# Optimization experiments

Measured on AMD Instinct MI355X. Metric: run time of the kernel, lower is better.

The kernel has to match this reference:

```python
import jax, jax.numpy as jnp
import numpy as np

DIM = 768
N_HEADS = 12
HEAD_DIM = DIM // N_HEADS
HIDDEN = 4 * DIM
EPS = 1e-5


def _layernorm(x, g, b):
    m = jnp.mean(x, axis=-1, keepdims=True)
    v = jnp.mean(jnp.square(x - m), axis=-1, keepdims=True)
    return (x - m) * jax.lax.rsqrt(v + EPS) * g + b


def setup_inputs() -> dict:
    key = jax.random.key(0)
    ks = jax.random.split(key, 16)
    s = lambda fan_in: 1.0 / np.sqrt(fan_in)
    return {
        "x": jax.random.normal(ks[0], (2, 2048, DIM), dtype=jnp.float32),
        "ln1_g": jnp.ones((DIM,), jnp.float32),
        "ln1_b": jnp.zeros((DIM,), jnp.float32),
        "qkv_w": jax.random.uniform(ks[1], (DIM, 3 * DIM), jnp.float32, -s(DIM), s(DIM)),
        "qkv_b": jax.random.uniform(ks[2], (3 * DIM,), jnp.float32, -s(DIM), s(DIM)),
        "proj_w": jax.random.uniform(ks[3], (DIM, DIM), jnp.float32, -s(DIM), s(DIM)),
        "proj_b": jax.random.uniform(ks[4], (DIM,), jnp.float32, -s(DIM), s(DIM)),
        "ln2_g": jnp.ones((DIM,), jnp.float32),
        "ln2_b": jnp.zeros((DIM,), jnp.float32),
        "w1": jax.random.uniform(ks[5], (DIM, HIDDEN), jnp.float32, -s(DIM), s(DIM)),
        "b1": jax.random.uniform(ks[6], (HIDDEN,), jnp.float32, -s(DIM), s(DIM)),
        "w2": jax.random.uniform(ks[7], (HIDDEN, DIM), jnp.float32, -s(HIDDEN), s(HIDDEN)),
        "b2": jax.random.uniform(ks[8], (DIM,), jnp.float32, -s(HIDDEN), s(HIDDEN)),
    }


def reference(x, ln1_g, ln1_b, qkv_w, qkv_b, proj_w, proj_b, ln2_g, ln2_b, w1, b1, w2, b2):
    B, N, C = x.shape
    # ---- attention branch (pre-norm) ----
    h = _layernorm(x, ln1_g, ln1_b)
    qkv = (h @ qkv_w + qkv_b).reshape(B, N, 3, N_HEADS, HEAD_DIM)
    qkv = qkv.transpose(2, 0, 3, 1, 4)  # [3, B, H, N, Dh]
    q, k, v = qkv[0], qkv[1], qkv[2]
    scale = HEAD_DIM ** -0.5
    scores = jnp.einsum("bhnd,bhmd->bhnm", q, k) * scale  # [B,H,N,N]
    attn = jax.nn.softmax(scores, axis=-1)
    ctx = jnp.einsum("bhnm,bhmd->bhnd", attn, v)  # [B,H,N,Dh]
    ctx = ctx.transpose(0, 2, 1, 3).reshape(B, N, C)
    x = x + ctx @ proj_w + proj_b
    # ---- MLP branch (pre-norm) ----
    h = _layernorm(x, ln2_g, ln2_b)
    h = jax.nn.gelu(h @ w1 + b1, approximate=False)  # torch nn.GELU default = exact erf
    x = x + h @ w2 + b2
    return x
```

## Files before the change

kernel.cpp:

```cpp
#include <hip/hip_runtime.h>
#include <hip/hip_bf16.h>
#include <math.h>

#define DIM 768
#define NHEADS 12
#define HDIM 64
#define HIDDEN 3072
#define SEQ 2048
#define NTOK 4096
#define QKV3 2304

typedef __attribute__((ext_vector_type(8))) __bf16 bf16x8;
typedef __attribute__((ext_vector_type(4))) float f32x4;
typedef __attribute__((ext_vector_type(16))) float f32x16;

__device__ __forceinline__ ushort f32_bf16(float f) {
  union { float f; uint u; } c{f};
  uint u = c.u;
  u = (u + 0x7FFFu + ((u >> 16) & 1u)) >> 16;
  return (ushort)u;
}

__device__ __forceinline__ float bf16_f32(ushort u) {
  union { uint u; float f; } c{(uint)u << 16};
  return c.f;
}

__device__ __forceinline__ uint cvt_pk_bf16(float lo, float hi) {
  uint r;
  asm("v_cvt_pk_bf16_f32 %0, %1, %2" : "=v"(r) : "v"(lo), "v"(hi));
  return r;
}

__device__ __forceinline__ void glds16(const ushort* g, ushort* l) {
  __builtin_amdgcn_global_load_lds(
      (const __attribute__((address_space(1))) unsigned int*)(const void*)g,
      (__attribute__((address_space(3))) unsigned int*)(void*)l, 16, 0, 0);
}

union U8 { uint u[4]; bf16x8 v; };

__global__ __launch_bounds__(256) void transpose_to_bf16(
    const float* __restrict__ in, ushort* __restrict__ out, int K, int N) {
  __shared__ float tile[32][33];
  int kb = blockIdx.y * 32, nb = blockIdx.x * 32;
  int tx = threadIdx.x, ty = threadIdx.y;
#pragma unroll
  for (int i = 0; i < 32; i += 8)
    tile[ty + i][tx] = in[(size_t)(kb + ty + i) * N + nb + tx];
  __syncthreads();
#pragma unroll
  for (int i = 0; i < 32; i += 8)
    out[(size_t)(nb + ty + i) * K + kb + tx] = f32_bf16(tile[tx][ty + i]);
}

__global__ __launch_bounds__(256) void ln_bf16(
    const float* __restrict__ x, const float* __restrict__ g,
    const float* __restrict__ bta, ushort* __restrict__ out) {
  int row = blockIdx.x;
  const float* xr = x + (size_t)row * DIM;
  int t = threadIdx.x;
  float v0 = xr[t], v1 = xr[t + 256], v2 = xr[t + 512];
  float s = v0 + v1 + v2;
  float q = v0 * v0 + v1 * v1 + v2 * v2;
#pragma unroll
  for (int m = 1; m < 64; m <<= 1) {
    s += __shfl_xor(s, m);
    q += __shfl_xor(q, m);
  }
  __shared__ float ss[4], qq[4];
  int wid = t >> 6;
  if ((t & 63) == 0) { ss[wid] = s; qq[wid] = q; }
  __syncthreads();
  s = ss[0] + ss[1] + ss[2] + ss[3];
  q = qq[0] + qq[1] + qq[2] + qq[3];
  float mean = s * (1.0f / DIM);
  float var = q * (1.0f / DIM) - mean * mean;
  float rs = rsqrtf(var + 1e-5f);
  size_t o = (size_t)row * DIM;
  out[o + t]       = f32_bf16((v0 - mean) * rs * g[t]       + bta[t]);
  out[o + t + 256] = f32_bf16((v1 - mean) * rs * g[t + 256] + bta[t + 256]);
  out[o + t + 512] = f32_bf16((v2 - mean) * rs * g[t + 512] + bta[t + 512]);
}

template <int EPI>
__global__ __launch_bounds__(256, 3) void gemm_bf16(
    const ushort* __restrict__ A, const ushort* __restrict__ Bt,
    const float* __restrict__ bias, const float* __restrict__ resid,
    void* __restrict__ outv, int M, int N, int K, int lda, int ldb,
    ushort* __restrict__ p0, ushort* __restrict__ p1, ushort* __restrict__ p2) {
  __shared__ __align__(16) ushort As[128 * 64];
  __shared__ __align__(16) ushort Bs[128 * 64];
  int t = threadIdx.x;
  int lane = t & 63, w = t >> 6;
  int wr = w >> 1, wc = w & 1;
  int m0 = blockIdx.y * 128, n0 = blockIdx.x * 128;
  int kb = blockIdx.z * K;
  f32x4 acc[4][4] = {};
  int rl = lane & 15, g = lane >> 4, rl7 = rl & 7;

  int baseRow = w * 32 + (lane >> 3);
  int cs = (lane & 7) ^ ((lane >> 3) & 7);
  const ushort* Asrc = A + (size_t)(m0 + baseRow) * lda + kb + cs * 8;
  const ushort* Bsrc = Bt + (size_t)(n0 + baseRow) * ldb + kb + cs * 8;
  ushort* Adst = &As[(w * 256 + lane) * 8];
  ushort* Bdst = &Bs[(w * 256 + lane) * 8];

  for (int k0 = 0; k0 < K; k0 += 64) {
    __syncthreads();
#pragma unroll
    for (int i = 0; i < 4; i++) {
      glds16(Asrc + (size_t)i * 8 * lda + k0, Adst + i * 512);
      glds16(Bsrc + (size_t)i * 8 * ldb + k0, Bdst + i * 512);
    }
    __syncthreads();
    bf16x8 a[2][4], b[2][4];
#pragma unroll
    for (int kk = 0; kk < 2; kk++)
#pragma unroll
      for (int i = 0; i < 4; i++) {
        a[kk][i] = *(const bf16x8*)&As[(wr * 64 + i * 16 + rl) * 64 + ((kk * 4 + g) ^ rl7) * 8];
        b[kk][i] = *(const bf16x8*)&Bs[(wc * 64 + i * 16 + rl) * 64 + ((kk * 4 + g) ^ rl7) * 8];
      }
#pragma unroll
    for (int kk = 0; kk < 2; kk++)
#pragma unroll
      for (int i = 0; i < 4; i++)
#pragma unroll
        for (int j = 0; j < 4; j++)
          acc[i][j] = __builtin_amdgcn_mfma_f32_16x16x32_bf16(a[kk][i], b[kk][j], acc[i][j], 0, 0, 0);
  }
  ushort* pz = (blockIdx.z == 0) ? p0 : ((blockIdx.z == 1) ? p1 : p2);
  int g4 = (lane >> 4) * 4;
#pragma unroll
  for (int i = 0; i < 4; i++) {
#pragma unroll
    for (int j = 0; j < 4; j++) {
      int col = n0 + wc * 64 + j * 16 + rl;
      float bval = (EPI == 3) ? 0.0f : bias[col];
#pragma unroll
      for (int r = 0; r < 4; r++) {
        int row = m0 + wr * 64 + i * 16 + g4 + r;
        float v = acc[i][j][r] + bval;
        if (EPI == 0) {
          ((ushort*)outv)[(size_t)row * N + col] = f32_bf16(v);
        } else if (EPI == 1) {
          v += resid[(size_t)row * N + col];
          ((float*)outv)[(size_t)row * N + col] = v;
        } else if (EPI == 2) {
          v = 0.5f * v * (1.0f + erff(v * 0.70710678118654752f));
          ((ushort*)outv)[(size_t)row * N + col] = f32_bf16(v);
        } else {
          pz[(size_t)row * N + col] = f32_bf16(v);
        }
      }
    }
  }
}

__global__ __launch_bounds__(256) void reduce3_kernel(
    const ushort* __restrict__ p0, const ushort* __restrict__ p1,
    const ushort* __restrict__ p2, const float* __restrict__ x1,
    const float* __restrict__ bias, float* __restrict__ out) {
  int i = blockIdx.x * 256 + threadIdx.x;
  int col = (i * 4) % DIM;
  const ushort4 a0 = ((const ushort4*)p0)[i];
  const ushort4 a1 = ((const ushort4*)p1)[i];
  const ushort4 a2 = ((const ushort4*)p2)[i];
  const float4 xv = ((const float4*)x1)[i];
  const float4 bv = *(const float4*)&bias[col];
  float4 o;
  o.x = xv.x + bv.x + bf16_f32(a0.x) + bf16_f32(a1.x) + bf16_f32(a2.x);
  o.y = xv.y + bv.y + bf16_f32(a0.y) + bf16_f32(a1.y) + bf16_f32(a2.y);
  o.z = xv.z + bv.z + bf16_f32(a0.z) + bf16_f32(a1.z) + bf16_f32(a2.z);
  o.w = xv.w + bv.w + bf16_f32(a0.w) + bf16_f32(a1.w) + bf16_f32(a2.w);
  ((float4*)out)[i] = o;
}

__global__ __launch_bounds__(256, 3) void attn_kernel(
    const ushort* __restrict__ qkv, ushort* __restrict__ ctx) {
  __shared__ __align__(16) ushort Ks[2][4096];
  __shared__ __align__(16) ushort Vt[2][4096];
  __shared__ float mml[2][2][64];
  int t = threadIdx.x, lane = t & 63, w = t >> 6;
  int qh = w & 1, kvpar = w >> 1;
  int kl = lane & 31, hi = lane >> 5;
  int qt = blockIdx.x, h = blockIdx.y, b = blockIdx.z;

  bf16x8 bq[4];
  {
    size_t qbase = (size_t)(b * SEQ + qt * 64 + qh * 32 + kl) * QKV3 + h * HDIM + hi * 8;
#pragma unroll
    for (int mi = 0; mi < 4; mi++) bq[mi] = *(const bf16x8*)(qkv + qbase + mi * 16);
  }
  f32x16 acc_o[2] = {};
  float m2 = -1e30f, lst = 0.0f;

  int pairLane = qh * 64 + lane;
  const ushort* kbase = qkv + (size_t)(b * SEQ) * QKV3 + DIM + h * HDIM;
  ushort* KsB = Ks[kvpar];
  ushort* VtB = Vt[kvpar];

  for (int it = 0; it < SEQ / 128; it++) {
    int kt = it * 2 + kvpar;
    __syncthreads();
#pragma unroll
    for (int i = 0; i < 4; i++) {
      int s = i * 128 + pairLane;
      int key = s >> 3, cc = s & 7;
      int c = cc ^ (key & 7);
      glds16(kbase + (size_t)(kt * 64 + key) * QKV3 + c * 8, &KsB[s * 8]);
    }
#pragma unroll
    for (int i = 0; i < 4; i++) {
      int s = i * 128 + pairLane;
      int key = s >> 3, c = s & 7;
      uint4 v4 = *(const uint4*)(kbase + DIM + (size_t)(kt * 64 + key) * QKV3 + c * 8);
      int co = ((key >> 3) ^ c) * 8 + (key & 7);
      uint vv[4] = {v4.x, v4.y, v4.z, v4.w};
#pragma unroll
      for (int u = 0; u < 4; u++) {
        VtB[(c * 8 + 2 * u) * 64 + co]     = (ushort)(vv[u] & 0xffffu);
        VtB[(c * 8 + 2 * u + 1) * 64 + co] = (ushort)(vv[u] >> 16);
      }
    }
    __syncthreads();

    f32x16 accs[2] = {};
    __builtin_amdgcn_s_setprio(1);
#pragma unroll
    for (int ks = 0; ks < 2; ks++) {
      int key = ks * 32 + kl;
      int kswz = key & 7;
#pragma unroll
      for (int mi = 0; mi < 4; mi++) {
        bf16x8 ak = *(const bf16x8*)&KsB[key * 64 + ((2 * mi + hi) ^ kswz) * 8];
        accs[ks] = __builtin_amdgcn_mfma_f32_32x32x16_bf16(ak, bq[mi], accs[ks], 0, 0, 0);
      }
    }
    __builtin_amdgcn_s_setprio(0);

    float mx = accs[0][0];
#pragma unroll
    for (int ks = 0; ks < 2; ks++)
#pragma unroll
      for (int r = 0; r < 16; r++) mx = fmaxf(mx, accs[ks][r]);
    mx = fmaxf(mx, __shfl_xor(mx, 32));
    float me = mx * 0.125f;
    if (!__all(me - m2 <= 8.0f)) {
      float newm = fmaxf(m2, me);
      float fac = __expf(m2 - newm);
      m2 = newm;
      lst *= fac;
#pragma unroll
      for (int r = 0; r < 16; r++) {
        int qrow = (r & 3) + 8 * (r >> 2) + 4 * hi;
        float fr = __shfl(fac, qrow | (lane & 32));
        acc_o[0][r] *= fr;
        acc_o[1][r] *= fr;
      }
    }
    float ps = 0.0f;
    uint PK[2][8];
#pragma unroll
    for (int ks = 0; ks < 2; ks++)
#pragma unroll
      for (int rp = 0; rp < 8; rp++) {
        float p0 = __expf(fmaf(accs[ks][2 * rp],     0.125f, -m2));
        float p1 = __expf(fmaf(accs[ks][2 * rp + 1], 0.125f, -m2));
        ps += p0 + p1;
        PK[ks][rp] = cvt_pk_bf16(p0, p1);
      }
    ps += __shfl_xor(ps, 32);
    lst += ps;

#pragma unroll
    for (int tt = 0; tt < 4; tt++) {
      const int ks = tt >> 1, tb = 4 * (tt & 1);
      uint e0 = hi ? PK[ks][tb]     : PK[ks][tb + 2];
      uint e1 = hi ? PK[ks][tb + 1] : PK[ks][tb + 3];
      uint x0 = __shfl_xor(e0, 32), x1 = __shfl_xor(e1, 32);
      uint l0 = hi ? PK[ks][tb + 2] : PK[ks][tb];
      uint l1 = hi ? PK[ks][tb + 3] : PK[ks][tb + 1];
      U8 a;
      a.u[0] = hi ? x0 : l0;
      a.u[1] = hi ? x1 : l1;
      a.u[2] = hi ? l0 : x0;
      a.u[3] = hi ? l1 : x1;
      __builtin_amdgcn_s_setprio(1);
#pragma unroll
      for (int dn = 0; dn < 2; dn++) {
        int d = dn * 32 + kl;
        bf16x8 bv = *(const bf16x8*)&VtB[d * 64 + ((2 * tt + hi) ^ (d >> 3)) * 8];
        acc_o[dn] = __builtin_amdgcn_mfma_f32_32x32x16_bf16(a.v, bv, acc_o[dn], 0, 0, 0);
      }
      __builtin_amdgcn_s_setprio(0);
    }
  }

  __syncthreads();
  float* obuf = (float*)(qh ? Ks[1] : Ks[0]);
  if (kvpar == 1) {
#pragma unroll
    for (int dn = 0; dn < 2; dn++)
#pragma unroll
      for (int r = 0; r < 16; r++)
        obuf[(dn * 16 + r) * 64 + lane] = acc_o[dn][r];
    mml[qh][0][lane] = m2;
    mml[qh][1][lane] = lst;
  }
  __syncthreads();
  if (kvpar == 0) {
    float mb = mml[qh][0][lane], lb = mml[qh][1][lane];
    float m = fmaxf(m2, mb);
    float fa = __expf(m2 - m), fb = __expf(mb - m);
    lst = lst * fa + lb * fb;
    float inv = 1.0f / lst;
#pragma unroll
    for (int r = 0; r < 16; r++) {
      int qrow = (r & 3) + 8 * (r >> 2) + 4 * hi;
      int src = qrow | (lane & 32);
      float far = __shfl(fa, src), fbr = __shfl(fb, src), ir = __shfl(inv, src);
      size_t row = (size_t)(b * SEQ + qt * 64 + qh * 32 + qrow);
#pragma unroll
      for (int dn = 0; dn < 2; dn++) {
        float v = (acc_o[dn][r] * far + obuf[(dn * 16 + r) * 64 + lane] * fbr) * ir;
        ctx[row * DIM + h * HDIM + dn * 32 + kl] = f32_bf16(v);
      }
    }
  }
}

extern "C" void kernel_launch(void* const* d_in, const int* in_sizes, int n_in,
                              void* d_out, int out_size, void* d_ws, size_t ws_size,
                              hipStream_t stream) {
  const float* x      = (const float*)d_in[0];
  const float* ln1_g  = (const float*)d_in[1];
  const float* ln1_b  = (const float*)d_in[2];
  const float* qkv_w  = (const float*)d_in[3];
  const float* qkv_b  = (const float*)d_in[4];
  const float* proj_w = (const float*)d_in[5];
  const float* proj_b = (const float*)d_in[6];
  const float* ln2_g  = (const float*)d_in[7];
  const float* ln2_b  = (const float*)d_in[8];
  const float* w1     = (const float*)d_in[9];
  const float* b1     = (const float*)d_in[10];
  const float* w2     = (const float*)d_in[11];
  const float* b2     = (const float*)d_in[12];
  float* out = (float*)d_out;

  char* ws = (char*)d_ws;
  size_t off = 0;
  auto alloc = [&](size_t bytes) -> void* {
    void* p = ws + off;
    off += (bytes + 255) & ~(size_t)255;
    return p;
  };
  ushort* wqkv_t  = (ushort*)alloc((size_t)QKV3 * DIM * 2);
  ushort* wproj_t = (ushort*)alloc((size_t)DIM * DIM * 2);
  ushort* w1_t    = (ushort*)alloc((size_t)HIDDEN * DIM * 2);
  ushort* w2_t    = (ushort*)alloc((size_t)DIM * HIDDEN * 2);
  ushort* hbuf    = (ushort*)alloc((size_t)NTOK * DIM * 2);
  ushort* ubuf    = (ushort*)alloc((size_t)NTOK * HIDDEN * 2);
  ushort* ctx     = (ushort*)alloc((size_t)NTOK * DIM * 2);
  float*  x1      = (float*)alloc((size_t)NTOK * DIM * 4);
  ushort* qkvbuf = ubuf;
  ushort* m1     = ubuf;
  ushort* part0 = (ushort*)ws;
  ushort* part1 = hbuf;
  ushort* part2 = ctx;

  transpose_to_bf16<<<dim3(QKV3 / 32, DIM / 32), dim3(32, 8), 0, stream>>>(qkv_w, wqkv_t, DIM, QKV3);
  transpose_to_bf16<<<dim3(DIM / 32, DIM / 32), dim3(32, 8), 0, stream>>>(proj_w, wproj_t, DIM, DIM);
  transpose_to_bf16<<<dim3(HIDDEN / 32, DIM / 32), dim3(32, 8), 0, stream>>>(w1, w1_t, DIM, HIDDEN);
  transpose_to_bf16<<<dim3(DIM / 32, HIDDEN / 32), dim3(32, 8), 0, stream>>>(w2, w2_t, HIDDEN, DIM);

  ln_bf16<<<NTOK, 256, 0, stream>>>(x, ln1_g, ln1_b, hbuf);
  gemm_bf16<0><<<dim3(QKV3 / 128, NTOK / 128), 256, 0, stream>>>(
      hbuf, wqkv_t, qkv_b, nullptr, qkvbuf, NTOK, QKV3, DIM, DIM, DIM,
      nullptr, nullptr, nullptr);
  attn_kernel<<<dim3(SEQ / 64, NHEADS, 2), 256, 0, stream>>>(qkvbuf, ctx);
  gemm_bf16<1><<<dim3(DIM / 128, NTOK / 128), 256, 0, stream>>>(
      ctx, wproj_t, proj_b, x, x1, NTOK, DIM, DIM, DIM, DIM,
      nullptr, nullptr, nullptr);
  ln_bf16<<<NTOK, 256, 0, stream>>>(x1, ln2_g, ln2_b, hbuf);
  gemm_bf16<2><<<dim3(HIDDEN / 128, NTOK / 128), 256, 0, stream>>>(
      hbuf, w1_t, b1, nullptr, m1, NTOK, HIDDEN, DIM, DIM, DIM,
      nullptr, nullptr, nullptr);
  gemm_bf16<3><<<dim3(DIM / 128, NTOK / 128, 3), 256, 0, stream>>>(
      m1, w2_t, nullptr, nullptr, nullptr, NTOK, DIM, HIDDEN / 3, HIDDEN, HIDDEN,
      part0, part1, part2);
  reduce3_kernel<<<NTOK * DIM / 4 / 256, 256, 0, stream>>>(
      part0, part1, part2, x1, b2, out);
}
```

Measured before the change: 199.1 us.

## Split attention KV loop across three wave pairs and merge weight transposes

The attention kernel goes from 256 to 384 threads, with three KV-parity wave pairs instead of two. Each pair handles every third KV tile, padded with dummy iterations, and the three partial softmax states are merged at the end. The exponentials are rewritten as exp2 with the scale folded in, the row-max reduction becomes a tree, and the s_setprio hints are removed. The four weight-transpose launches are fused into one kernel to cut launch overhead. The dummy iterations and the larger shared-memory footprint may reduce occupancy.

```diff
diff --git a/kernel.cpp b/kernel.cpp
--- a/kernel.cpp
+++ b/kernel.cpp
@@ -9,6 +9,7 @@
 #define SEQ 2048
 #define NTOK 4096
 #define QKV3 2304
+#define KVT 32
 
 typedef __attribute__((ext_vector_type(8))) __bf16 bf16x8;
 typedef __attribute__((ext_vector_type(4))) float f32x4;
@@ -40,10 +41,20 @@
 
 union U8 { uint u[4]; bf16x8 v; };
 
-__global__ __launch_bounds__(256) void transpose_to_bf16(
-    const float* __restrict__ in, ushort* __restrict__ out, int K, int N) {
+__global__ __launch_bounds__(256) void transpose_all(
+    const float* __restrict__ qkv_w, const float* __restrict__ proj_w,
+    const float* __restrict__ w1, const float* __restrict__ w2,
+    ushort* __restrict__ o0, ushort* __restrict__ o1,
+    ushort* __restrict__ o2, ushort* __restrict__ o3) {
   __shared__ float tile[32][33];
-  int kb = blockIdx.y * 32, nb = blockIdx.x * 32;
+  int bid = blockIdx.x;
+  const float* in; ushort* out; int K, N;
+  if (bid < 1728)      { in = qkv_w;  out = o0; K = DIM;    N = QKV3; }
+  else if (bid < 2304) { bid -= 1728; in = proj_w; out = o1; K = DIM;  N = DIM; }
+  else if (bid < 4608) { bid -= 2304; in = w1;  out = o2; K = DIM;    N = HIDDEN; }
+  else                 { bid -= 4608; in = w2;  out = o3; K = HIDDEN; N = DIM; }
+  int ntx = N / 32;
+  int nb = (bid % ntx) * 32, kb = (bid / ntx) * 32;
   int tx = threadIdx.x, ty = threadIdx.y;
 #pragma unroll
   for (int i = 0; i < 32; i += 8)
@@ -177,15 +188,14 @@
   ((float4*)out)[i] = o;
 }
 
-__global__ __launch_bounds__(256, 3) void attn_kernel(
+__global__ __launch_bounds__(384, 4) void attn_kernel(
     const ushort* __restrict__ qkv, ushort* __restrict__ ctx) {
-  __shared__ __align__(16) ushort Ks[2][4096];
-  __shared__ __align__(16) ushort Vt[2][4096];
-  __shared__ float mml[2][2][64];
+  __shared__ __align__(16) ushort SH[6 * 4096];
   int t = threadIdx.x, lane = t & 63, w = t >> 6;
   int qh = w & 1, kvpar = w >> 1;
   int kl = lane & 31, hi = lane >> 5;
   int qt = blockIdx.x, h = blockIdx.y, b = blockIdx.z;
+  const float SCL2 = 0.18033688f;
 
   bf16x8 bq[4];
   {
@@ -198,36 +208,40 @@
 
   int pairLane = qh * 64 + lane;
   const ushort* kbase = qkv + (size_t)(b * SEQ) * QKV3 + DIM + h * HDIM;
-  ushort* KsB = Ks[kvpar];
-  ushort* VtB = Vt[kvpar];
-
-  for (int it = 0; it < SEQ / 128; it++) {
-    int kt = it * 2 + kvpar;
+  ushort* KsB = SH + kvpar * 4096;
+  ushort* VtB = SH + (3 + kvpar) * 4096;
+
+  for (int it = 0; it < 11; it++) {
+    int kt = it * 3 + kvpar;
+    bool dummy = (kt >= KVT);
+    if (dummy) kt = KVT - 1;
     __syncthreads();
-#pragma unroll
-    for (int i = 0; i < 4; i++) {
-      int s = i * 128 + pairLane;
-      int key = s >> 3, cc = s & 7;
-      int c = cc ^ (key & 7);
-      glds16(kbase + (size_t)(kt * 64 + key) * QKV3 + c * 8, &KsB[s * 8]);
-    }
-#pragma unroll
-    for (int i = 0; i < 4; i++) {
-      int s = i * 128 + pairLane;
-      int key = s >> 3, c = s & 7;
-      uint4 v4 = *(const uint4*)(kbase + DIM + (size_t)(kt * 64 + key) * QKV3 + c * 8);
-      int co = ((key >> 3) ^ c) * 8 + (key & 7);
-      uint vv[4] = {v4.x, v4.y, v4.z, v4.w};
-#pragma unroll
-      for (int u = 0; u < 4; u++) {
-        VtB[(c * 8 + 2 * u) * 64 + co]     = (ushort)(vv[u] & 0xffffu);
-        VtB[(c * 8 + 2 * u + 1) * 64 + co] = (ushort)(vv[u] >> 16);
+    if (!dummy) {
+#pragma unroll
+      for (int i = 0; i < 4; i++) {
+        int s = i * 128 + pairLane;
+        int key = s >> 3, cc = s & 7;
+        int c = cc ^ (key & 7);
+        glds16(kbase + (size_t)(kt * 64 + key) * QKV3 + c * 8, &KsB[s * 8]);
+      }
+#pragma unroll
+      for (int i = 0; i < 4; i++) {
+        int s = i * 128 + pairLane;
+        int key = s >> 3, c = s & 7;
+        uint4 v4 = *(const uint4*)(kbase + DIM + (size_t)(kt * 64 + key) * QKV3 + c * 8);
+        int co = ((key >> 3) ^ c) * 8 + (key & 7);
+        uint vv[4] = {v4.x, v4.y, v4.z, v4.w};
+#pragma unroll
+        for (int u = 0; u < 4; u++) {
+          VtB[(c * 8 + 2 * u) * 64 + co]     = (ushort)(vv[u] & 0xffffu);
+          VtB[(c * 8 + 2 * u + 1) * 64 + co] = (ushort)(vv[u] >> 16);
+        }
       }
     }
     __syncthreads();
+    if (dummy) continue;
 
     f32x16 accs[2] = {};
-    __builtin_amdgcn_s_setprio(1);
 #pragma unroll
     for (int ks = 0; ks < 2; ks++) {
       int key = ks * 32 + kl;
@@ -238,18 +252,20 @@
         accs[ks] = __builtin_amdgcn_mfma_f32_32x32x16_bf16(ak, bq[mi], accs[ks], 0, 0, 0);
       }
     }
-    __builtin_amdgcn_s_setprio(0);
-
-    float mx = accs[0][0];
-#pragma unroll
-    for (int ks = 0; ks < 2; ks++)
-#pragma unroll
-      for (int r = 0; r < 16; r++) mx = fmaxf(mx, accs[ks][r]);
-    mx = fmaxf(mx, __shfl_xor(mx, 32));
-    float me = mx * 0.125f;
-    if (!__all(me - m2 <= 8.0f)) {
-      float newm = fmaxf(m2, me);
-      float fac = __expf(m2 - newm);
+
+    float tm[8];
+#pragma unroll
+    for (int i = 0; i < 8; i++)
+      tm[i] = fmaxf(fmaxf(accs[0][i], accs[0][i + 8]), fmaxf(accs[1][i], accs[1][i + 8]));
+#pragma unroll
+    for (int s = 4; s > 0; s >>= 1)
+#pragma unroll
+      for (int i = 0; i < s; i++) tm[i] = fmaxf(tm[i], tm[i + s]);
+    float mx = fmaxf(tm[0], __shfl_xor(tm[0], 32));
+    float me2 = mx * SCL2;
+    if (!__all(me2 - m2 <= 11.5f)) {
+      float newm = fmaxf(m2, me2);
+      float fac = exp2f(m2 - newm);
       m2 = newm;
       lst *= fac;
 #pragma unroll
@@ -266,8 +282,8 @@
     for (int ks = 0; ks < 2; ks++)
 #pragma unroll
       for (int rp = 0; rp < 8; rp++) {
-        float p0 = __expf(fmaf(accs[ks][2 * rp],     0.125f, -m2));
-        float p1 = __expf(fmaf(accs[ks][2 * rp + 1], 0.125f, -m2));
+        float p0 = exp2f(fmaf(accs[ks][2 * rp],     SCL2, -m2));
+        float p1 = exp2f(fmaf(accs[ks][2 * rp + 1], SCL2, -m2));
         ps += p0 + p1;
         PK[ks][rp] = cvt_pk_bf16(p0, p1);
       }
@@ -287,44 +303,51 @@
       a.u[1] = hi ? x1 : l1;
       a.u[2] = hi ? l0 : x0;
       a.u[3] = hi ? l1 : x1;
-      __builtin_amdgcn_s_setprio(1);
 #pragma unroll
       for (int dn = 0; dn < 2; dn++) {
         int d = dn * 32 + kl;
         bf16x8 bv = *(const bf16x8*)&VtB[d * 64 + ((2 * tt + hi) ^ (d >> 3)) * 8];
         acc_o[dn] = __builtin_amdgcn_mfma_f32_32x32x16_bf16(a.v, bv, acc_o[dn], 0, 0, 0);
       }
-      __builtin_amdgcn_s_setprio(0);
     }
   }
 
   __syncthreads();
-  float* obuf = (float*)(qh ? Ks[1] : Ks[0]);
-  if (kvpar == 1) {
+  float* obuf = (float*)SH;
+  float* mml  = (float*)(SH + 4 * 4096);
+  if (kvpar > 0) {
+    float* ob = obuf + (size_t)(qh * 2 + kvpar - 1) * 2048;
 #pragma unroll
     for (int dn = 0; dn < 2; dn++)
 #pragma unroll
       for (int r = 0; r < 16; r++)
-        obuf[(dn * 16 + r) * 64 + lane] = acc_o[dn][r];
-    mml[qh][0][lane] = m2;
-    mml[qh][1][lane] = lst;
+        ob[(dn * 16 + r) * 64 + lane] = acc_o[dn][r];
+    mml[((qh * 2 + kvpar - 1) * 2 + 0) * 64 + lane] = m2;
+    mml[((qh * 2 + kvpar - 1) * 2 + 1) * 64 + lane] = lst;
   }
   __syncthreads();
   if (kvpar == 0) {
-    float mb = mml[qh][0][lane], lb = mml[qh][1][lane];
-    float m = fmaxf(m2, mb);
-    float fa = __expf(m2 - m), fb = __expf(mb - m);
-    lst = lst * fa + lb * fb;
-    float inv = 1.0f / lst;
+    float ma = mml[((qh * 2 + 0) * 2 + 0) * 64 + lane];
+    float la = mml[((qh * 2 + 0) * 2 + 1) * 64 + lane];
+    float mb = mml[((qh * 2 + 1) * 2 + 0) * 64 + lane];
+    float lb = mml[((qh * 2 + 1) * 2 + 1) * 64 + lane];
+    float m = fmaxf(m2, fmaxf(ma, mb));
+    float f0 = exp2f(m2 - m), fa = exp2f(ma - m), fb = exp2f(mb - m);
+    float ltot = lst * f0 + la * fa + lb * fb;
+    float inv = 1.0f / ltot;
+    const float* oa = obuf + (size_t)(qh * 2 + 0) * 2048;
+    const float* ob = obuf + (size_t)(qh * 2 + 1) * 2048;
 #pragma unroll
     for (int r = 0; r < 16; r++) {
       int qrow = (r & 3) + 8 * (r >> 2) + 4 * hi;
       int src = qrow | (lane & 32);
-      float far = __shfl(fa, src), fbr = __shfl(fb, src), ir = __shfl(inv, src);
+      float f0r = __shfl(f0, src), far = __shfl(fa, src), fbr = __shfl(fb, src);
+      float ir = __shfl(inv, src);
       size_t row = (size_t)(b * SEQ + qt * 64 + qh * 32 + qrow);
 #pragma unroll
       for (int dn = 0; dn < 2; dn++) {
-        float v = (acc_o[dn][r] * far + obuf[(dn * 16 + r) * 64 + lane] * fbr) * ir;
+        float v = (acc_o[dn][r] * f0r + oa[(dn * 16 + r) * 64 + lane] * far
+                   + ob[(dn * 16 + r) * 64 + lane] * fbr) * ir;
         ctx[row * DIM + h * HDIM + dn * 32 + kl] = f32_bf16(v);
       }
     }
@@ -370,16 +393,14 @@
   ushort* part1 = hbuf;
   ushort* part2 = ctx;
 
-  transpose_to_bf16<<<dim3(QKV3 / 32, DIM / 32), dim3(32, 8), 0, stream>>>(qkv_w, wqkv_t, DIM, QKV3);
-  transpose_to_bf16<<<dim3(DIM / 32, DIM / 32), dim3(32, 8), 0, stream>>>(proj_w, wproj_t, DIM, DIM);
-  transpose_to_bf16<<<dim3(HIDDEN / 32, DIM / 32), dim3(32, 8), 0, stream>>>(w1, w1_t, DIM, HIDDEN);
-  transpose_to_bf16<<<dim3(DIM / 32, HIDDEN / 32), dim3(32, 8), 0, stream>>>(w2, w2_t, HIDDEN, DIM);
+  transpose_all<<<6912, dim3(32, 8), 0, stream>>>(
+      qkv_w, proj_w, w1, w2, wqkv_t, wproj_t, w1_t, w2_t);
 
   ln_bf16<<<NTOK, 256, 0, stream>>>(x, ln1_g, ln1_b, hbuf);
   gemm_bf16<0><<<dim3(QKV3 / 128, NTOK / 128), 256, 0, stream>>>(
       hbuf, wqkv_t, qkv_b, nullptr, qkvbuf, NTOK, QKV3, DIM, DIM, DIM,
       nullptr, nullptr, nullptr);
-  attn_kernel<<<dim3(SEQ / 64, NHEADS, 2), 256, 0, stream>>>(qkvbuf, ctx);
+  attn_kernel<<<dim3(SEQ / 64, NHEADS, 2), 384, 0, stream>>>(qkvbuf, ctx);
   gemm_bf16<1><<<dim3(DIM / 128, NTOK / 128), 256, 0, stream>>>(
       ctx, wproj_t, proj_b, x, x1, NTOK, DIM, DIM, DIM, DIM,
       nullptr, nullptr, nullptr);
```

Measured after the change: 256.7 us. +28.9%, slower.

## Merge weight transposes, swizzle GEMM tiles, use exp2 softmax in attention

Applied to the files above, without the earlier changes.

Fuses the four weight transpose launches into one kernel that picks its matrix by flat block id, cutting launch overhead. The GEMM remaps block indices with a stride-8 swizzle so co-resident blocks share operand tiles in cache. The attention kernel folds log2(e) into the score scale to use exp2 directly, computes the row max as a tree reduction to shorten the dependency chain, and drops the s_setprio hints. These are independent tweaks; the swizzle could also hurt L2 locality, and removing the priority hints may change how waves interleave.

```diff
diff --git a/kernel.cpp b/kernel.cpp
--- a/kernel.cpp
+++ b/kernel.cpp
@@ -40,10 +40,20 @@
 
 union U8 { uint u[4]; bf16x8 v; };
 
-__global__ __launch_bounds__(256) void transpose_to_bf16(
-    const float* __restrict__ in, ushort* __restrict__ out, int K, int N) {
+__global__ __launch_bounds__(256) void transpose_all(
+    const float* __restrict__ qkv_w, const float* __restrict__ proj_w,
+    const float* __restrict__ w1, const float* __restrict__ w2,
+    ushort* __restrict__ o0, ushort* __restrict__ o1,
+    ushort* __restrict__ o2, ushort* __restrict__ o3) {
   __shared__ float tile[32][33];
-  int kb = blockIdx.y * 32, nb = blockIdx.x * 32;
+  int bid = blockIdx.x;
+  const float* in; ushort* out; int K, N;
+  if (bid < 1728)      { in = qkv_w;  out = o0; K = DIM;    N = QKV3; }
+  else if (bid < 2304) { bid -= 1728; in = proj_w; out = o1; K = DIM;  N = DIM; }
+  else if (bid < 4608) { bid -= 2304; in = w1;  out = o2; K = DIM;    N = HIDDEN; }
+  else                 { bid -= 4608; in = w2;  out = o3; K = HIDDEN; N = DIM; }
+  int ntx = N / 32;
+  int nb = (bid % ntx) * 32, kb = (bid / ntx) * 32;
   int tx = threadIdx.x, ty = threadIdx.y;
 #pragma unroll
   for (int i = 0; i < 32; i += 8)
@@ -94,7 +104,10 @@
   int t = threadIdx.x;
   int lane = t & 63, w = t >> 6;
   int wr = w >> 1, wc = w & 1;
-  int m0 = blockIdx.y * 128, n0 = blockIdx.x * 128;
+  int nxy = gridDim.x * gridDim.y;
+  int flat = blockIdx.x + gridDim.x * blockIdx.y;
+  int swz = (flat & 7) * (nxy >> 3) + (flat >> 3);
+  int m0 = (swz / gridDim.x) * 128, n0 = (swz % gridDim.x) * 128;
   int kb = blockIdx.z * K;
   f32x4 acc[4][4] = {};
   int rl = lane & 15, g = lane >> 4, rl7 = rl & 7;
@@ -186,6 +199,7 @@
   int qh = w & 1, kvpar = w >> 1;
   int kl = lane & 31, hi = lane >> 5;
   int qt = blockIdx.x, h = blockIdx.y, b = blockIdx.z;
+  const float SCL2 = 0.18033688f;
 
   bf16x8 bq[4];
   {
@@ -227,7 +241,6 @@
     __syncthreads();
 
     f32x16 accs[2] = {};
-    __builtin_amdgcn_s_setprio(1);
 #pragma unroll
     for (int ks = 0; ks < 2; ks++) {
       int key = ks * 32 + kl;
@@ -238,18 +251,20 @@
         accs[ks] = __builtin_amdgcn_mfma_f32_32x32x16_bf16(ak, bq[mi], accs[ks], 0, 0, 0);
       }
     }
-    __builtin_amdgcn_s_setprio(0);
-
-    float mx = accs[0][0];
-#pragma unroll
-    for (int ks = 0; ks < 2; ks++)
-#pragma unroll
-      for (int r = 0; r < 16; r++) mx = fmaxf(mx, accs[ks][r]);
-    mx = fmaxf(mx, __shfl_xor(mx, 32));
-    float me = mx * 0.125f;
-    if (!__all(me - m2 <= 8.0f)) {
-      float newm = fmaxf(m2, me);
-      float fac = __expf(m2 - newm);
+
+    float tm[8];
+#pragma unroll
+    for (int i = 0; i < 8; i++)
+      tm[i] = fmaxf(fmaxf(accs[0][i], accs[0][i + 8]), fmaxf(accs[1][i], accs[1][i + 8]));
+#pragma unroll
+    for (int s = 4; s > 0; s >>= 1)
+#pragma unroll
+      for (int i = 0; i < s; i++) tm[i] = fmaxf(tm[i], tm[i + s]);
+    float mx = fmaxf(tm[0], __shfl_xor(tm[0], 32));
+    float me2 = mx * SCL2;
+    if (!__all(me2 - m2 <= 11.5f)) {
+      float newm = fmaxf(m2, me2);
+      float fac = exp2f(m2 - newm);
       m2 = newm;
       lst *= fac;
 #pragma unroll
@@ -266,8 +281,8 @@
     for (int ks = 0; ks < 2; ks++)
 #pragma unroll
       for (int rp = 0; rp < 8; rp++) {
-        float p0 = __expf(fmaf(accs[ks][2 * rp],     0.125f, -m2));
-        float p1 = __expf(fmaf(accs[ks][2 * rp + 1], 0.125f, -m2));
+        float p0 = exp2f(fmaf(accs[ks][2 * rp],     SCL2, -m2));
+        float p1 = exp2f(fmaf(accs[ks][2 * rp + 1], SCL2, -m2));
         ps += p0 + p1;
         PK[ks][rp] = cvt_pk_bf16(p0, p1);
       }
@@ -287,14 +302,12 @@
       a.u[1] = hi ? x1 : l1;
       a.u[2] = hi ? l0 : x0;
       a.u[3] = hi ? l1 : x1;
-      __builtin_amdgcn_s_setprio(1);
 #pragma unroll
       for (int dn = 0; dn < 2; dn++) {
         int d = dn * 32 + kl;
         bf16x8 bv = *(const bf16x8*)&VtB[d * 64 + ((2 * tt + hi) ^ (d >> 3)) * 8];
         acc_o[dn] = __builtin_amdgcn_mfma_f32_32x32x16_bf16(a.v, bv, acc_o[dn], 0, 0, 0);
       }
-      __builtin_amdgcn_s_setprio(0);
     }
   }
 
@@ -313,7 +326,7 @@
   if (kvpar == 0) {
     float mb = mml[qh][0][lane], lb = mml[qh][1][lane];
     float m = fmaxf(m2, mb);
-    float fa = __expf(m2 - m), fb = __expf(mb - m);
+    float fa = exp2f(m2 - m), fb = exp2f(mb - m);
     lst = lst * fa + lb * fb;
     float inv = 1.0f / lst;
 #pragma unroll
@@ -370,10 +383,8 @@
   ushort* part1 = hbuf;
   ushort* part2 = ctx;
 
-  transpose_to_bf16<<<dim3(QKV3 / 32, DIM / 32), dim3(32, 8), 0, stream>>>(qkv_w, wqkv_t, DIM, QKV3);
-  transpose_to_bf16<<<dim3(DIM / 32, DIM / 32), dim3(32, 8), 0, stream>>>(proj_w, wproj_t, DIM, DIM);
-  transpose_to_bf16<<<dim3(HIDDEN / 32, DIM / 32), dim3(32, 8), 0, stream>>>(w1, w1_t, DIM, HIDDEN);
-  transpose_to_bf16<<<dim3(DIM / 32, HIDDEN / 32), dim3(32, 8), 0, stream>>>(w2, w2_t, HIDDEN, DIM);
+  transpose_all<<<6912, dim3(32, 8), 0, stream>>>(
+      qkv_w, proj_w, w1, w2, wqkv_t, wproj_t, w1_t, w2_t);
 
   ln_bf16<<<NTOK, 256, 0, stream>>>(x, ln1_g, ln1_b, hbuf);
   gemm_bf16<0><<<dim3(QKV3 / 128, NTOK / 128), 256, 0, stream>>>(
```

Result: no change. 196.3 us (-1.4%).
